# Performance work log

Measured on AMD Instinct MI355X. Metric: run time of the kernel, lower is better.

## Reference

```python
import jax, jax.numpy as jnp
import numpy as np

HIDDEN = 128
OUT_EMB = 256
OUT_CH = 1
NUM_LAYERS = 3
NUM_EDGES = 1000000
NUM_NODES = 50000


def glorot_orthogonal(key, shape, scale=2.0):
    # orthogonal init then rescale variance like DIG's glorot_orthogonal
    W = jax.nn.initializers.orthogonal()(key, shape, jnp.float32)
    W = W * jnp.sqrt(scale / ((shape[0] + shape[1]) * jnp.var(W)))
    return W


def setup_inputs() -> dict:
    key = jax.random.key(0)
    ks = jax.random.split(key, 8)
    e2 = jax.random.normal(ks[0], (NUM_EDGES, HIDDEN), dtype=jnp.float32)
    i = jax.random.randint(ks[1], (NUM_EDGES,), 0, NUM_NODES, dtype=jnp.int64)
    W_up = glorot_orthogonal(ks[2], (OUT_EMB, HIDDEN))
    b_up = jnp.zeros((OUT_EMB,), jnp.float32)
    Ws = jnp.stack([glorot_orthogonal(k, (OUT_EMB, OUT_EMB)) for k in jax.random.split(ks[3], NUM_LAYERS)])
    bs = jnp.zeros((NUM_LAYERS, OUT_EMB), jnp.float32)
    W_out = glorot_orthogonal(ks[4], (OUT_CH, OUT_EMB))
    return {"e2": e2, "i": i, "W_up": W_up, "b_up": b_up,
            "Ws": Ws, "bs": bs, "W_out": W_out, "num_nodes": NUM_NODES}


def reference(e2, i, W_up, b_up, Ws, bs, W_out, num_nodes):
    # scatter-sum edge messages into nodes: v[n] = sum_{k: i[k]==n} e2[k]
    v = jax.ops.segment_sum(e2, i, num_segments=num_nodes)  # [N, HIDDEN]
    v = v @ W_up.T + b_up                                   # [N, OUT_EMB]
    for l in range(NUM_LAYERS):
        v = jax.nn.silu(v @ Ws[l].T + bs[l])
    return v @ W_out.T                                      # [N, OUT_CH]
```

## Files before the change

### kernel.cpp

```cpp
#include <hip/hip_runtime.h>

#define HIDDEN 128
#define OUT_EMB 256
#define NLAYERS 3
#define TM 64
#define LDA 264

typedef __bf16 bf16x8 __attribute__((ext_vector_type(8)));
typedef float f32x4 __attribute__((ext_vector_type(4)));

__device__ __forceinline__ unsigned short f2bf(float x) {
    union { float f; unsigned u; } c; c.f = x;
    unsigned r = c.u + 0x7fff + ((c.u >> 16) & 1);
    return (unsigned short)(r >> 16);
}
__device__ __forceinline__ float bf2f(unsigned short h) {
    union { unsigned u; float f; } c; c.u = ((unsigned)h) << 16;
    return c.f;
}

__global__ __launch_bounds__(256) void hist_kernel(
    const int* __restrict__ idx, int* __restrict__ counts, int ne)
{
    int e = blockIdx.x * 256 + threadIdx.x;
    if (e < ne) atomicAdd(&counts[idx[e]], 1);
}

__global__ __launch_bounds__(256) void scan1_kernel(
    const int* __restrict__ counts, int* __restrict__ bsum, int n)
{
    __shared__ int sh[256];
    int t = threadIdx.x;
    int i = blockIdx.x * 256 + t;
    sh[t] = (i < n) ? counts[i] : 0;
    __syncthreads();
    for (int off = 128; off > 0; off >>= 1) {
        if (t < off) sh[t] += sh[t + off];
        __syncthreads();
    }
    if (t == 0) bsum[blockIdx.x] = sh[0];
}

__global__ __launch_bounds__(256) void scan2_kernel(
    int* __restrict__ bsum, int* __restrict__ boff, int nb)
{
    __shared__ int sh[256];
    int t = threadIdx.x;
    int v = (t < nb) ? bsum[t] : 0;
    sh[t] = v;
    __syncthreads();
    for (int off = 1; off < 256; off <<= 1) {
        int u = (t >= off) ? sh[t - off] : 0;
        __syncthreads();
        sh[t] += u;
        __syncthreads();
    }
    if (t < nb) boff[t] = sh[t] - v;
}

__global__ __launch_bounds__(256) void scan3_kernel(
    const int* __restrict__ counts, const int* __restrict__ boff,
    int* __restrict__ offsets, int* __restrict__ cursor, int n)
{
    __shared__ int sh[256];
    int t = threadIdx.x;
    int i = blockIdx.x * 256 + t;
    int v = (i < n) ? counts[i] : 0;
    sh[t] = v;
    __syncthreads();
    for (int off = 1; off < 256; off <<= 1) {
        int u = (t >= off) ? sh[t - off] : 0;
        __syncthreads();
        sh[t] += u;
        __syncthreads();
    }
    if (i < n) {
        int excl = boff[blockIdx.x] + sh[t] - v;
        offsets[i] = excl;
        cursor[i]  = excl;
    }
}

__global__ __launch_bounds__(256) void fill_kernel(
    const int* __restrict__ idx, int* __restrict__ cursor,
    int* __restrict__ edge_list, int ne)
{
    int e = blockIdx.x * 256 + threadIdx.x;
    if (e < ne) {
        int pos = atomicAdd(&cursor[idx[e]], 1);
        edge_list[pos] = e;
    }
}

__global__ __launch_bounds__(256) void gather_kernel(
    const float* __restrict__ e2, const int* __restrict__ edge_list,
    const int* __restrict__ offsets, const int* __restrict__ counts,
    unsigned short* __restrict__ vbf, int Mpad)
{
    int node = blockIdx.x * 4 + (threadIdx.x >> 6);
    if (node >= Mpad) return;
    int lane = threadIdx.x & 63;
    int half = lane >> 5;
    int c4   = lane & 31;
    int start = offsets[node];
    int cnt   = counts[node];

    f32x4 a0 = {0.f, 0.f, 0.f, 0.f};
    f32x4 a1 = {0.f, 0.f, 0.f, 0.f};

    int j = 0;
    for (; j + 4 <= cnt; j += 4) {
        int e0 = edge_list[start + j + half];
        int e1 = edge_list[start + j + 2 + half];
        f32x4 x0 = *(const f32x4*)(e2 + (long long)e0 * HIDDEN + c4 * 4);
        f32x4 x1 = *(const f32x4*)(e2 + (long long)e1 * HIDDEN + c4 * 4);
        a0 += x0;
        a1 += x1;
    }
    for (; j + 2 <= cnt; j += 2) {
        int e0 = edge_list[start + j + half];
        f32x4 x0 = *(const f32x4*)(e2 + (long long)e0 * HIDDEN + c4 * 4);
        a0 += x0;
    }
    if (j < cnt && half == 0) {
        int e0 = edge_list[start + j];
        f32x4 x0 = *(const f32x4*)(e2 + (long long)e0 * HIDDEN + c4 * 4);
        a1 += x0;
    }
    a0 += a1;
    a0[0] += __shfl_xor(a0[0], 32);
    a0[1] += __shfl_xor(a0[1], 32);
    a0[2] += __shfl_xor(a0[2], 32);
    a0[3] += __shfl_xor(a0[3], 32);

    if (half == 0) {
        unsigned lo = (unsigned)f2bf(a0[0]) | ((unsigned)f2bf(a0[1]) << 16);
        unsigned hi = (unsigned)f2bf(a0[2]) | ((unsigned)f2bf(a0[3]) << 16);
        uint2 p; p.x = lo; p.y = hi;
        *(uint2*)(vbf + (long long)node * HIDDEN + c4 * 4) = p;
    }
}

__global__ __launch_bounds__(256) void convert_kernel(
    const float* __restrict__ wup_f, const float* __restrict__ ws_f,
    unsigned short* __restrict__ wup, unsigned short* __restrict__ wsl)
{
    int t = blockIdx.x * blockDim.x + threadIdx.x;
    const int n1 = OUT_EMB * HIDDEN;
    const int n2 = NLAYERS * OUT_EMB * OUT_EMB;
    if (t < n1) wup[t] = f2bf(wup_f[t]);
    else if (t < n1 + n2) wsl[t - n1] = f2bf(ws_f[t - n1]);
}

__global__ __launch_bounds__(256) void mlp_kernel(
    const unsigned short* __restrict__ vbf,
    const unsigned short* __restrict__ wup,
    const float* __restrict__ bup,
    const unsigned short* __restrict__ wsl,
    const float* __restrict__ bs,
    const float* __restrict__ wout,
    float* __restrict__ out, int M)
{
    __shared__ unsigned short act[TM * LDA];

    const int tid  = threadIdx.x;
    const int wv   = tid >> 6;
    const int lane = tid & 63;
    const int ln15 = lane & 15;
    const int kq   = lane >> 4;
    const int n0   = wv * 64;
    const long long rowbase = (long long)blockIdx.x * TM;

    f32x4 acc[4][4];

    #pragma unroll
    for (int mt = 0; mt < 4; ++mt)
        #pragma unroll
        for (int nt = 0; nt < 4; ++nt)
            acc[mt][nt] = (f32x4){0.f, 0.f, 0.f, 0.f};

    #pragma unroll
    for (int ks = 0; ks < 4; ++ks) {
        bf16x8 a[4], b[4];
        #pragma unroll
        for (int mt = 0; mt < 4; ++mt)
            a[mt] = *(const bf16x8*)&vbf[(rowbase + mt * 16 + ln15) * HIDDEN + ks * 32 + kq * 8];
        #pragma unroll
        for (int nt = 0; nt < 4; ++nt)
            b[nt] = *(const bf16x8*)&wup[(n0 + nt * 16 + ln15) * HIDDEN + ks * 32 + kq * 8];
        #pragma unroll
        for (int mt = 0; mt < 4; ++mt)
            #pragma unroll
            for (int nt = 0; nt < 4; ++nt)
                acc[mt][nt] = __builtin_amdgcn_mfma_f32_16x16x32_bf16(a[mt], b[nt], acc[mt][nt], 0, 0, 0);
    }
    #pragma unroll
    for (int nt = 0; nt < 4; ++nt) {
        int n = n0 + nt * 16 + ln15;
        float bias = bup[n];
        #pragma unroll
        for (int mt = 0; mt < 4; ++mt)
            #pragma unroll
            for (int r = 0; r < 4; ++r)
                act[(mt * 16 + kq * 4 + r) * LDA + n] = f2bf(acc[mt][nt][r] + bias);
    }
    __syncthreads();

    for (int l = 0; l < NLAYERS; ++l) {
        const unsigned short* W = wsl + l * OUT_EMB * OUT_EMB;
        const float* bias_l = bs + l * OUT_EMB;

        #pragma unroll
        for (int mt = 0; mt < 4; ++mt)
            #pragma unroll
            for (int nt = 0; nt < 4; ++nt)
                acc[mt][nt] = (f32x4){0.f, 0.f, 0.f, 0.f};

        #pragma unroll
        for (int ks = 0; ks < 8; ++ks) {
            bf16x8 a[4], b[4];
            #pragma unroll
            for (int mt = 0; mt < 4; ++mt)
                a[mt] = *(const bf16x8*)&act[(mt * 16 + ln15) * LDA + ks * 32 + kq * 8];
            #pragma unroll
            for (int nt = 0; nt < 4; ++nt)
                b[nt] = *(const bf16x8*)&W[(n0 + nt * 16 + ln15) * OUT_EMB + ks * 32 + kq * 8];
            #pragma unroll
            for (int mt = 0; mt < 4; ++mt)
                #pragma unroll
                for (int nt = 0; nt < 4; ++nt)
                    acc[mt][nt] = __builtin_amdgcn_mfma_f32_16x16x32_bf16(a[mt], b[nt], acc[mt][nt], 0, 0, 0);
        }
        __syncthreads();
        #pragma unroll
        for (int nt = 0; nt < 4; ++nt) {
            int n = n0 + nt * 16 + ln15;
            float bias = bias_l[n];
            #pragma unroll
            for (int mt = 0; mt < 4; ++mt)
                #pragma unroll
                for (int r = 0; r < 4; ++r) {
                    float x = acc[mt][nt][r] + bias;
                    float s = x / (1.f + __expf(-x));
                    act[(mt * 16 + kq * 4 + r) * LDA + n] = f2bf(s);
                }
        }
        __syncthreads();
    }

    {
        int r = tid >> 2;
        int part = tid & 3;
        const unsigned short* arow = &act[r * LDA + part * 64];
        const float* wrow = wout + part * 64;
        float s = 0.f;
        #pragma unroll
        for (int jj = 0; jj < 64; ++jj) s += bf2f(arow[jj]) * wrow[jj];
        s += __shfl_xor(s, 1);
        s += __shfl_xor(s, 2);
        long long rowg = rowbase + r;
        if (part == 0 && rowg < M) out[rowg] = s;
    }
}

extern "C" void kernel_launch(void* const* d_in, const int* in_sizes, int n_in,
                              void* d_out, int out_size, void* d_ws, size_t ws_size,
                              hipStream_t stream) {
    const float* e2    = (const float*)d_in[0];
    const int*   idx   = (const int*)d_in[1];
    const float* W_up  = (const float*)d_in[2];
    const float* b_up  = (const float*)d_in[3];
    const float* Ws    = (const float*)d_in[4];
    const float* bs    = (const float*)d_in[5];
    const float* W_out = (const float*)d_in[6];

    const int ne = in_sizes[0] / HIDDEN;
    const int M  = out_size;
    const int Mpad = ((M + TM - 1) / TM) * TM;
    const int nb = (Mpad + 255) / 256;

    char* p = (char*)d_ws;
    unsigned short* vbf    = (unsigned short*)p;  p += (size_t)Mpad * HIDDEN * 2;
    unsigned short* wup_bf = (unsigned short*)p;  p += (size_t)OUT_EMB * HIDDEN * 2;
    unsigned short* wsl_bf = (unsigned short*)p;  p += (size_t)NLAYERS * OUT_EMB * OUT_EMB * 2;
    int* counts    = (int*)p;  p += (size_t)Mpad * 4;
    int* offsets   = (int*)p;  p += (size_t)Mpad * 4;
    int* cursor    = (int*)p;  p += (size_t)Mpad * 4;
    int* bsum      = (int*)p;  p += 256 * 4;
    int* boff      = (int*)p;  p += 256 * 4;
    int* edge_list = (int*)p;  p += (size_t)ne * 4;

    hipMemsetAsync(counts, 0, (size_t)Mpad * 4, stream);

    hist_kernel <<<(ne + 255) / 256, 256, 0, stream>>>(idx, counts, ne);
    scan1_kernel<<<nb, 256, 0, stream>>>(counts, bsum, Mpad);
    scan2_kernel<<<1, 256, 0, stream>>>(bsum, boff, nb);
    scan3_kernel<<<nb, 256, 0, stream>>>(counts, boff, offsets, cursor, Mpad);
    fill_kernel <<<(ne + 255) / 256, 256, 0, stream>>>(idx, cursor, edge_list, ne);

    {
        int total = OUT_EMB * HIDDEN + NLAYERS * OUT_EMB * OUT_EMB;
        convert_kernel<<<(total + 255) / 256, 256, 0, stream>>>(W_up, Ws, wup_bf, wsl_bf);
    }

    gather_kernel<<<(Mpad + 3) / 4, 256, 0, stream>>>(e2, edge_list, offsets, counts, vbf, Mpad);

    mlp_kernel<<<Mpad / TM, 256, 0, stream>>>(vbf, wup_bf, b_up, wsl_bf, bs, W_out,
                                              (float*)d_out, M);
}
```

Before: 890.5 us.

## Fuse weight conversion into histogram, nontemporal gather loads, transposed MFMA epilogue

Merges the weight bf16 conversion kernel into the histogram kernel as extra blocks, removing one launch, and vectorises the conversion to 4 elements per thread. The gather loads of e2 become nontemporal, since each row is read once. The MLP swaps the MFMA operands so each lane holds 4 consecutive output columns, which lets bias be read as a vector and activations be written as packed 8-byte LDS stores instead of scalar 2-byte stores. Most of the time is likely in the gather, so the gain hinges on the nontemporal hint, which may also change cache behaviour in unexpected ways.

```diff
diff --git a/kernel.cpp b/kernel.cpp
--- a/kernel.cpp
+++ b/kernel.cpp
@@ -18,12 +18,34 @@
     union { unsigned u; float f; } c; c.u = ((unsigned)h) << 16;
     return c.f;
 }
-
-__global__ __launch_bounds__(256) void hist_kernel(
-    const int* __restrict__ idx, int* __restrict__ counts, int ne)
-{
-    int e = blockIdx.x * 256 + threadIdx.x;
-    if (e < ne) atomicAdd(&counts[idx[e]], 1);
+__device__ __forceinline__ unsigned pack2(float a, float b) {
+    return (unsigned)f2bf(a) | ((unsigned)f2bf(b) << 16);
+}
+
+__global__ __launch_bounds__(256) void hist_convert_kernel(
+    const int* __restrict__ idx, int* __restrict__ counts, int ne, int nbh,
+    const float* __restrict__ wup_f, const float* __restrict__ ws_f,
+    unsigned short* __restrict__ wup, unsigned short* __restrict__ wsl)
+{
+    if ((int)blockIdx.x < nbh) {
+        int e = blockIdx.x * 256 + threadIdx.x;
+        if (e < ne) atomicAdd(&counts[idx[e]], 1);
+    } else {
+        const int n1 = OUT_EMB * HIDDEN;
+        const int n2 = NLAYERS * OUT_EMB * OUT_EMB;
+        int t = (blockIdx.x - nbh) * 256 + threadIdx.x;
+        int base = t * 4;
+        if (base < n1) {
+            f32x4 x = *(const f32x4*)(wup_f + base);
+            uint2 p; p.x = pack2(x[0], x[1]); p.y = pack2(x[2], x[3]);
+            *(uint2*)(wup + base) = p;
+        } else if (base < n1 + n2) {
+            int j = base - n1;
+            f32x4 x = *(const f32x4*)(ws_f + j);
+            uint2 p; p.x = pack2(x[0], x[1]); p.y = pack2(x[2], x[3]);
+            *(uint2*)(wsl + j) = p;
+        }
+    }
 }
 
 __global__ __launch_bounds__(256) void scan1_kernel(
@@ -112,19 +134,19 @@
     for (; j + 4 <= cnt; j += 4) {
         int e0 = edge_list[start + j + half];
         int e1 = edge_list[start + j + 2 + half];
-        f32x4 x0 = *(const f32x4*)(e2 + (long long)e0 * HIDDEN + c4 * 4);
-        f32x4 x1 = *(const f32x4*)(e2 + (long long)e1 * HIDDEN + c4 * 4);
+        f32x4 x0 = __builtin_nontemporal_load((const f32x4*)(e2 + (long long)e0 * HIDDEN + c4 * 4));
+        f32x4 x1 = __builtin_nontemporal_load((const f32x4*)(e2 + (long long)e1 * HIDDEN + c4 * 4));
         a0 += x0;
         a1 += x1;
     }
     for (; j + 2 <= cnt; j += 2) {
         int e0 = edge_list[start + j + half];
-        f32x4 x0 = *(const f32x4*)(e2 + (long long)e0 * HIDDEN + c4 * 4);
+        f32x4 x0 = __builtin_nontemporal_load((const f32x4*)(e2 + (long long)e0 * HIDDEN + c4 * 4));
         a0 += x0;
     }
     if (j < cnt && half == 0) {
         int e0 = edge_list[start + j];
-        f32x4 x0 = *(const f32x4*)(e2 + (long long)e0 * HIDDEN + c4 * 4);
+        f32x4 x0 = __builtin_nontemporal_load((const f32x4*)(e2 + (long long)e0 * HIDDEN + c4 * 4));
         a1 += x0;
     }
     a0 += a1;
@@ -134,22 +156,9 @@
     a0[3] += __shfl_xor(a0[3], 32);
 
     if (half == 0) {
-        unsigned lo = (unsigned)f2bf(a0[0]) | ((unsigned)f2bf(a0[1]) << 16);
-        unsigned hi = (unsigned)f2bf(a0[2]) | ((unsigned)f2bf(a0[3]) << 16);
-        uint2 p; p.x = lo; p.y = hi;
+        uint2 p; p.x = pack2(a0[0], a0[1]); p.y = pack2(a0[2], a0[3]);
         *(uint2*)(vbf + (long long)node * HIDDEN + c4 * 4) = p;
     }
-}
-
-__global__ __launch_bounds__(256) void convert_kernel(
-    const float* __restrict__ wup_f, const float* __restrict__ ws_f,
-    unsigned short* __restrict__ wup, unsigned short* __restrict__ wsl)
-{
-    int t = blockIdx.x * blockDim.x + threadIdx.x;
-    const int n1 = OUT_EMB * HIDDEN;
-    const int n2 = NLAYERS * OUT_EMB * OUT_EMB;
-    if (t < n1) wup[t] = f2bf(wup_f[t]);
-    else if (t < n1 + n2) wsl[t - n1] = f2bf(ws_f[t - n1]);
 }
 
 __global__ __launch_bounds__(256) void mlp_kernel(
@@ -181,28 +190,33 @@
 
     #pragma unroll
     for (int ks = 0; ks < 4; ++ks) {
-        bf16x8 a[4], b[4];
+        bf16x8 a[4], w[4];
         #pragma unroll
         for (int mt = 0; mt < 4; ++mt)
             a[mt] = *(const bf16x8*)&vbf[(rowbase + mt * 16 + ln15) * HIDDEN + ks * 32 + kq * 8];
         #pragma unroll
         for (int nt = 0; nt < 4; ++nt)
-            b[nt] = *(const bf16x8*)&wup[(n0 + nt * 16 + ln15) * HIDDEN + ks * 32 + kq * 8];
+            w[nt] = *(const bf16x8*)&wup[(n0 + nt * 16 + ln15) * HIDDEN + ks * 32 + kq * 8];
         #pragma unroll
         for (int mt = 0; mt < 4; ++mt)
             #pragma unroll
             for (int nt = 0; nt < 4; ++nt)
-                acc[mt][nt] = __builtin_amdgcn_mfma_f32_16x16x32_bf16(a[mt], b[nt], acc[mt][nt], 0, 0, 0);
+                acc[mt][nt] = __builtin_amdgcn_mfma_f32_16x16x32_bf16(w[nt], a[mt], acc[mt][nt], 0, 0, 0);
     }
     #pragma unroll
     for (int nt = 0; nt < 4; ++nt) {
-        int n = n0 + nt * 16 + ln15;
-        float bias = bup[n];
-        #pragma unroll
-        for (int mt = 0; mt < 4; ++mt)
-            #pragma unroll
-            for (int r = 0; r < 4; ++r)
-                act[(mt * 16 + kq * 4 + r) * LDA + n] = f2bf(acc[mt][nt][r] + bias);
+        int nb4 = n0 + nt * 16 + kq * 4;
+        f32x4 bi = *(const f32x4*)(bup + nb4);
+        #pragma unroll
+        for (int mt = 0; mt < 4; ++mt) {
+            int row = mt * 16 + ln15;
+            float x0 = acc[mt][nt][0] + bi[0];
+            float x1 = acc[mt][nt][1] + bi[1];
+            float x2 = acc[mt][nt][2] + bi[2];
+            float x3 = acc[mt][nt][3] + bi[3];
+            uint2 p; p.x = pack2(x0, x1); p.y = pack2(x2, x3);
+            *(uint2*)&act[row * LDA + nb4] = p;
+        }
     }
     __syncthreads();
 
@@ -218,32 +232,38 @@
 
         #pragma unroll
         for (int ks = 0; ks < 8; ++ks) {
-            bf16x8 a[4], b[4];
+            bf16x8 a[4], w[4];
             #pragma unroll
             for (int mt = 0; mt < 4; ++mt)
                 a[mt] = *(const bf16x8*)&act[(mt * 16 + ln15) * LDA + ks * 32 + kq * 8];
             #pragma unroll
             for (int nt = 0; nt < 4; ++nt)
-                b[nt] = *(const bf16x8*)&W[(n0 + nt * 16 + ln15) * OUT_EMB + ks * 32 + kq * 8];
+                w[nt] = *(const bf16x8*)&W[(n0 + nt * 16 + ln15) * OUT_EMB + ks * 32 + kq * 8];
             #pragma unroll
             for (int mt = 0; mt < 4; ++mt)
                 #pragma unroll
                 for (int nt = 0; nt < 4; ++nt)
-                    acc[mt][nt] = __builtin_amdgcn_mfma_f32_16x16x32_bf16(a[mt], b[nt], acc[mt][nt], 0, 0, 0);
+                    acc[mt][nt] = __builtin_amdgcn_mfma_f32_16x16x32_bf16(w[nt], a[mt], acc[mt][nt], 0, 0, 0);
         }
         __syncthreads();
         #pragma unroll
         for (int nt = 0; nt < 4; ++nt) {
-            int n = n0 + nt * 16 + ln15;
-            float bias = bias_l[n];
-            #pragma unroll
-            for (int mt = 0; mt < 4; ++mt)
-                #pragma unroll
-                for (int r = 0; r < 4; ++r) {
-                    float x = acc[mt][nt][r] + bias;
-                    float s = x / (1.f + __expf(-x));
-                    act[(mt * 16 + kq * 4 + r) * LDA + n] = f2bf(s);
-                }
+            int nb4 = n0 + nt * 16 + kq * 4;
+            f32x4 bi = *(const f32x4*)(bias_l + nb4);
+            #pragma unroll
+            for (int mt = 0; mt < 4; ++mt) {
+                int row = mt * 16 + ln15;
+                float x0 = acc[mt][nt][0] + bi[0];
+                float x1 = acc[mt][nt][1] + bi[1];
+                float x2 = acc[mt][nt][2] + bi[2];
+                float x3 = acc[mt][nt][3] + bi[3];
+                x0 = x0 / (1.f + __expf(-x0));
+                x1 = x1 / (1.f + __expf(-x1));
+                x2 = x2 / (1.f + __expf(-x2));
+                x3 = x3 / (1.f + __expf(-x3));
+                uint2 p; p.x = pack2(x0, x1); p.y = pack2(x2, x3);
+                *(uint2*)&act[row * LDA + nb4] = p;
+            }
         }
         __syncthreads();
     }
@@ -292,17 +312,18 @@
 
     hipMemsetAsync(counts, 0, (size_t)Mpad * 4, stream);
 
-    hist_kernel <<<(ne + 255) / 256, 256, 0, stream>>>(idx, counts, ne);
+    {
+        const int nbh = (ne + 255) / 256;
+        const int total4 = (OUT_EMB * HIDDEN + NLAYERS * OUT_EMB * OUT_EMB) / 4;
+        const int nbc = (total4 + 255) / 256;
+        hist_convert_kernel<<<nbh + nbc, 256, 0, stream>>>(
+            idx, counts, ne, nbh, W_up, Ws, wup_bf, wsl_bf);
+    }
     scan1_kernel<<<nb, 256, 0, stream>>>(counts, bsum, Mpad);
     scan2_kernel<<<1, 256, 0, stream>>>(bsum, boff, nb);
     scan3_kernel<<<nb, 256, 0, stream>>>(counts, boff, offsets, cursor, Mpad);
     fill_kernel <<<(ne + 255) / 256, 256, 0, stream>>>(idx, cursor, edge_list, ne);
 
-    {
-        int total = OUT_EMB * HIDDEN + NLAYERS * OUT_EMB * OUT_EMB;
-        convert_kernel<<<(total + 255) / 256, 256, 0, stream>>>(W_up, Ws, wup_bf, wsl_bf);
-    }
-
     gather_kernel<<<(Mpad + 3) / 4, 256, 0, stream>>>(e2, edge_list, offsets, counts, vbf, Mpad);
 
     mlp_kernel<<<Mpad / TM, 256, 0, stream>>>(vbf, wup_bf, b_up, wsl_bf, bs, W_out,
```

Measured after the change: 849.2 us. 4.6% less time.
